# Kernel optimization log

Hardware: AMD Instinct MI355X
Metric: run time of the kernel (lower is better)

## Reference

```python
import jax, jax.numpy as jnp
import numpy as np

IN_DIMS = 512
TOKEN_DIM = 512
NUM_HEADS = 1
D = TOKEN_DIM * NUM_HEADS
SCALE = TOKEN_DIM ** (-0.5)
EPS = 1e-12  # torch F.normalize default


def _l2norm(v, axis):
    n = jnp.sqrt(jnp.sum(v * v, axis=axis, keepdims=True))
    return v / jnp.maximum(n, EPS)


def setup_inputs() -> dict:
    key = jax.random.key(0)
    ks = jax.random.split(key, 10)
    B, C, H, W = 64, IN_DIMS, 28, 28
    s_in = IN_DIMS ** -0.5
    s_d = D ** -0.5
    return {
        "x": jax.random.normal(ks[0], (B, C, H, W), jnp.float32),
        "Wq": jax.random.normal(ks[1], (IN_DIMS, D), jnp.float32) * s_in,
        "bq": jax.random.normal(ks[2], (D,), jnp.float32) * 0.01,
        "Wk": jax.random.normal(ks[3], (IN_DIMS, D), jnp.float32) * s_in,
        "bk": jax.random.normal(ks[4], (D,), jnp.float32) * 0.01,
        "w_g": jax.random.normal(ks[5], (D, 1), jnp.float32),
        "Wp": jax.random.normal(ks[6], (D, D), jnp.float32) * s_d,
        "bp": jax.random.normal(ks[7], (D,), jnp.float32) * 0.01,
        "Wf": jax.random.normal(ks[8], (D, TOKEN_DIM), jnp.float32) * s_d,
        "bf": jax.random.normal(ks[9], (TOKEN_DIM,), jnp.float32) * 0.01,
    }


def reference(x, Wq, bq, Wk, bk, w_g, Wp, bp, Wf, bf):
    B, C, H, W = x.shape
    t = x.reshape(B, C, H * W).transpose(0, 2, 1)          # [B, N, C]
    query = _l2norm(t @ Wq + bq, axis=-1)                  # [B, N, D]
    k = _l2norm(t @ Wk + bk, axis=-1)                      # [B, N, D]
    attn = _l2norm((query @ w_g) * SCALE, axis=1)          # [B, N, 1], normalized over tokens
    ctx = jnp.sum(attn * query, axis=1, keepdims=True)     # [B, 1, D] global context
    out = (ctx * k) @ Wp + bp + query                      # [B, N, D]
    out = out @ Wf + bf                                    # [B, N, TOKEN_DIM]
    return out.transpose(0, 2, 1).reshape(B, -1, H, W)
```

## Files before the change

### kernel.cpp

```cpp
#include <hip/hip_runtime.h>

#define EPSN 1e-12f
#define SCALE_F 0.044194173824159216f
#define MTOT 50176

typedef __bf16 bf16x8 __attribute__((ext_vector_type(8)));
typedef float  f32x4  __attribute__((ext_vector_type(4)));

__device__ __forceinline__ void gld16(const void* src, void* dst) {
  __builtin_amdgcn_global_load_lds(
      (const __attribute__((address_space(1))) unsigned int*)src,
      (__attribute__((address_space(3))) unsigned int*)dst, 16, 0, 0);
}

__global__ __launch_bounds__(256) void k_xt(const float* __restrict__ x,
                                            __bf16* __restrict__ xT, int b0) {
  __shared__ float T[32][33];
  const int n0 = blockIdx.x * 32, c0 = blockIdx.y * 32;
  const int bl = blockIdx.z, b = b0 + bl;
  const int dx = threadIdx.x, ty = threadIdx.y;
  #pragma unroll
  for (int pp = 0; pp < 4; ++pp) {
    int c = ty + pp * 8;
    int n = n0 + dx;
    T[c][dx] = (n < 784) ? x[((size_t)b * 512 + c0 + c) * 784 + n] : 0.f;
  }
  __syncthreads();
  #pragma unroll
  for (int pp = 0; pp < 4; ++pp) {
    int n = ty + pp * 8;
    if (n0 + n < 784)
      xT[((size_t)bl * 784 + n0 + n) * 512 + c0 + dx] = (__bf16)T[dx][n];
  }
}

__global__ __launch_bounds__(256) void k_prep_t(const float* __restrict__ Wq,
                                                const float* __restrict__ Wk,
                                                __bf16* __restrict__ WqT,
                                                __bf16* __restrict__ WkT) {
  __shared__ float Tq[32][33], Tk[32][33];
  const int c0 = blockIdx.x * 32, d0 = blockIdx.y * 32;
  const int dx = threadIdx.x, cy = threadIdx.y;
  #pragma unroll
  for (int p = 0; p < 4; ++p) {
    int c = cy + p * 8;
    Tq[c][dx] = Wq[(size_t)(c0 + c) * 512 + d0 + dx];
    Tk[c][dx] = Wk[(size_t)(c0 + c) * 512 + d0 + dx];
  }
  __syncthreads();
  #pragma unroll
  for (int p = 0; p < 4; ++p) {
    int d = cy + p * 8;
    WqT[(size_t)(d0 + d) * 512 + c0 + dx] = (__bf16)Tq[dx][d];
    WkT[(size_t)(d0 + d) * 512 + c0 + dx] = (__bf16)Tk[dx][d];
  }
}

__global__ __launch_bounds__(512) void k_prep_w(const float* __restrict__ Wp,
                                                const float* __restrict__ Wf,
                                                const float* __restrict__ bp,
                                                const float* __restrict__ bfv,
                                                __bf16* __restrict__ WcT,
                                                float* __restrict__ bpf) {
  const int kk0 = blockIdx.x * 2;
  const int d = threadIdx.x;
  float acc0 = 0.f, acc1 = 0.f, bacc = 0.f;
  const bool dobp = (blockIdx.x == 0);
  for (int c = 0; c < 512; ++c) {
    float wf = Wf[(size_t)c * 512 + d];
    acc0 = fmaf(Wp[(size_t)kk0 * 512 + c],       wf, acc0);
    acc1 = fmaf(Wp[(size_t)(kk0 + 1) * 512 + c], wf, acc1);
    if (dobp) bacc = fmaf(bp[c], wf, bacc);
  }
  WcT[(size_t)d * 1024 + kk0]           = (__bf16)acc0;
  WcT[(size_t)d * 1024 + kk0 + 1]       = (__bf16)acc1;
  WcT[(size_t)d * 1024 + 512 + kk0]     = (__bf16)Wf[(size_t)kk0 * 512 + d];
  WcT[(size_t)d * 1024 + 512 + kk0 + 1] = (__bf16)Wf[(size_t)(kk0 + 1) * 512 + d];
  if (dobp) bpf[d] = bacc + bfv[d];
}

__global__ __launch_bounds__(256, 2) void k_gemm(const __bf16* __restrict__ xT,
                                                 const __bf16* __restrict__ WqT,
                                                 const __bf16* __restrict__ WkT,
                                                 const float* __restrict__ bq,
                                                 const float* __restrict__ bk,
                                                 const float* __restrict__ wg,
                                                 const int b0,
                                                 __bf16* __restrict__ qraw,
                                                 __bf16* __restrict__ kraw,
                                                 float* __restrict__ psqQ,
                                                 float* __restrict__ psqK,
                                                 float* __restrict__ gdo) {
  __shared__ __align__(1024) unsigned char stg[3][24576];
  const int t = threadIdx.x, l = t & 63, w = t >> 6;
  const int li = l & 15, lq = l >> 4;
  const int p = blockIdx.x;
  const int xq = p & 7, q2 = p >> 3;
  const int nt = q2 & 3;
  const int g = (q2 >> 2) * 8 + xq;
  const int bl = g / 7, mt = g % 7;
  const int b = b0 + bl;
  const int m0 = mt * 128;

  const int r0 = 2 * w, r1 = r0 + 1;
  int row0 = m0 + r0 * 16 + li; if (row0 > 783) row0 = 783;
  int row1 = m0 + r1 * 16 + li; if (row1 > 783) row1 = 783;
  const __bf16* a0s = xT + ((size_t)bl * 784 + row0) * 512 + lq * 8;
  const __bf16* a1s = xT + ((size_t)bl * 784 + row1) * 512 + lq * 8;
  const __bf16* q0s = WqT + (size_t)(nt * 128 + r0 * 16 + li) * 512 + lq * 8;
  const __bf16* q1s = WqT + (size_t)(nt * 128 + r1 * 16 + li) * 512 + lq * 8;
  const __bf16* k0s = WkT + (size_t)(nt * 128 + r0 * 16 + li) * 512 + lq * 8;
  const __bf16* k1s = WkT + (size_t)(nt * 128 + r1 * 16 + li) * 512 + lq * 8;

  f32x4 accQ[4][4] = {}, accK[4][4] = {};

  auto stage = [&](unsigned char* buf, int ks) {
    const int kk = (ks > 15 ? 15 : ks) * 32;
    gld16(a0s + kk, buf + r0 * 1024);
    gld16(a1s + kk, buf + r1 * 1024);
    gld16(q0s + kk, buf + 8192 + r0 * 1024);
    gld16(q1s + kk, buf + 8192 + r1 * 1024);
    gld16(k0s + kk, buf + 16384 + r0 * 1024);
    gld16(k1s + kk, buf + 16384 + r1 * 1024);
  };
  auto mstep = [&](const unsigned char* buf) {
    bf16x8 af[4];
    #pragma unroll
    for (int rb = 0; rb < 4; ++rb)
      af[rb] = *(const bf16x8*)(buf + ((w & 1) * 4 + rb) * 1024 + l * 16);
    #pragma unroll
    for (int cb = 0; cb < 4; ++cb) {
      bf16x8 bq8 = *(const bf16x8*)(buf + 8192 + ((w >> 1) * 4 + cb) * 1024 + l * 16);
      #pragma unroll
      for (int rb = 0; rb < 4; ++rb)
        accQ[rb][cb] = __builtin_amdgcn_mfma_f32_16x16x32_bf16(af[rb], bq8, accQ[rb][cb], 0, 0, 0);
      bf16x8 bk8 = *(const bf16x8*)(buf + 16384 + ((w >> 1) * 4 + cb) * 1024 + l * 16);
      #pragma unroll
      for (int rb = 0; rb < 4; ++rb)
        accK[rb][cb] = __builtin_amdgcn_mfma_f32_16x16x32_bf16(af[rb], bk8, accK[rb][cb], 0, 0, 0);
    }
  };

  unsigned char *bc = stg[0], *bn = stg[1], *bn2 = stg[2];
  stage(bc, 0); stage(bn, 1);
  asm volatile("s_waitcnt vmcnt(6)" ::: "memory");
  __builtin_amdgcn_s_barrier();
  __builtin_amdgcn_sched_barrier(0);
  #pragma unroll 1
  for (int ks = 0; ks < 16; ++ks) {
    stage(bn2, ks + 2);
    __builtin_amdgcn_sched_barrier(0);
    mstep(bc);
    asm volatile("s_waitcnt vmcnt(6)" ::: "memory");
    __builtin_amdgcn_s_barrier();
    __builtin_amdgcn_sched_barrier(0);
    unsigned char* tmp = bc; bc = bn; bn = bn2; bn2 = tmp;
  }
  asm volatile("s_waitcnt vmcnt(0)" ::: "memory");

  const int colb = nt * 128 + (w >> 1) * 64;
  const int cg = nt * 2 + (w >> 1);
  float bqv[4], bkv[4], wv[4];
  #pragma unroll
  for (int cb = 0; cb < 4; ++cb) {
    int col = colb + cb * 16 + li;
    bqv[cb] = bq[col]; bkv[cb] = bk[col]; wv[cb] = wg[col];
  }
  #pragma unroll
  for (int rb = 0; rb < 4; ++rb)
    #pragma unroll
    for (int j = 0; j < 4; ++j) {
      int rowg = m0 + (w & 1) * 64 + rb * 16 + lq * 4 + j;
      bool ok = rowg < 784;
      size_t token = (size_t)b * 784 + rowg;
      float ssq = 0.f, ssk = 0.f, sg = 0.f;
      #pragma unroll
      for (int cb = 0; cb < 4; ++cb) {
        float vq = accQ[rb][cb][j] + bqv[cb];
        float vk = accK[rb][cb][j] + bkv[cb];
        ssq = fmaf(vq, vq, ssq);
        ssk = fmaf(vk, vk, ssk);
        sg  = fmaf(vq, wv[cb], sg);
        if (ok) {
          qraw[token * 512 + colb + cb * 16 + li] = (__bf16)vq;
          kraw[token * 512 + colb + cb * 16 + li] = (__bf16)vk;
        }
      }
      ssq += __shfl_xor(ssq, 1); ssq += __shfl_xor(ssq, 2); ssq += __shfl_xor(ssq, 4); ssq += __shfl_xor(ssq, 8);
      ssk += __shfl_xor(ssk, 1); ssk += __shfl_xor(ssk, 2); ssk += __shfl_xor(ssk, 4); ssk += __shfl_xor(ssk, 8);
      sg  += __shfl_xor(sg, 1);  sg  += __shfl_xor(sg, 2);  sg  += __shfl_xor(sg, 4);  sg  += __shfl_xor(sg, 8);
      if (ok && li == 0) {
        psqQ[(size_t)cg * MTOT + token] = ssq;
        psqK[(size_t)cg * MTOT + token] = ssk;
        gdo [(size_t)cg * MTOT + token] = sg;
      }
    }
}

__global__ __launch_bounds__(256) void k_normc(const float* __restrict__ psqQ,
                                               const float* __restrict__ psqK,
                                               const float* __restrict__ gdo,
                                               float* __restrict__ invqA,
                                               float* __restrict__ invkA,
                                               float* __restrict__ coefA,
                                               float* __restrict__ gA) {
  const int tkn = blockIdx.x * 256 + threadIdx.x;
  if (tkn >= MTOT) return;
  float sq = 0.f, sk = 0.f, gd = 0.f;
  #pragma unroll
  for (int cg = 0; cg < 8; ++cg) {
    sq += psqQ[(size_t)cg * MTOT + tkn];
    sk += psqK[(size_t)cg * MTOT + tkn];
    gd += gdo[(size_t)cg * MTOT + tkn];
  }
  float invq = 1.f / fmaxf(sqrtf(sq), EPSN);
  float invk = 1.f / fmaxf(sqrtf(sk), EPSN);
  float gv = gd * invq;
  invqA[tkn] = invq;
  invkA[tkn] = invk;
  coefA[tkn] = gv * invq;
  gA[tkn]    = gv;
}

__global__ __launch_bounds__(512) void k_pctx(const __bf16* __restrict__ qraw,
                                              const float* __restrict__ coefA,
                                              const float* __restrict__ gA,
                                              float* __restrict__ ctx) {
  __shared__ float wred[8];
  __shared__ float part[4][128];
  const int ch = blockIdx.x, b = blockIdx.y, t = threadIdx.x;
  const size_t base = (size_t)b * 784;
  float gsq;
  { float gv = gA[base + t]; gsq = gv * gv; }
  if (t + 512 < 784) { float gv = gA[base + t + 512]; gsq = fmaf(gv, gv, gsq); }
  gsq += __shfl_xor(gsq, 1);  gsq += __shfl_xor(gsq, 2);  gsq += __shfl_xor(gsq, 4);
  gsq += __shfl_xor(gsq, 8);  gsq += __shfl_xor(gsq, 16); gsq += __shfl_xor(gsq, 32);
  if ((t & 63) == 0) wred[t >> 6] = gsq;
  __syncthreads();
  float tot = 0.f;
  #pragma unroll
  for (int i = 0; i < 8; ++i) tot += wred[i];
  const float alpha = SCALE_F / fmaxf(sqrtf(tot) * SCALE_F, EPSN);
  const int dof = t & 127, s = t >> 7;
  const int nb = s * 196;
  const __bf16* qb = qraw + (base + nb) * 512 + ch * 128 + dof;
  const float* cf = coefA + base + nb;
  float a0 = 0.f, a1 = 0.f, a2 = 0.f, a3 = 0.f;
  for (int n = 0; n < 196; n += 4) {
    a0 = fmaf(cf[n],     (float)qb[(size_t)n * 512],       a0);
    a1 = fmaf(cf[n + 1], (float)qb[(size_t)(n + 1) * 512], a1);
    a2 = fmaf(cf[n + 2], (float)qb[(size_t)(n + 2) * 512], a2);
    a3 = fmaf(cf[n + 3], (float)qb[(size_t)(n + 3) * 512], a3);
  }
  part[s][dof] = (a0 + a1) + (a2 + a3);
  __syncthreads();
  if (t < 128) {
    float sum = part[0][t] + part[1][t] + part[2][t] + part[3][t];
    ctx[(size_t)b * 512 + ch * 128 + t] = alpha * sum;
  }
}

__global__ __launch_bounds__(256, 3) void k_out(const __bf16* __restrict__ qraw,
                                                const __bf16* __restrict__ kraw,
                                                const float* __restrict__ invqA,
                                                const float* __restrict__ invkA,
                                                const float* __restrict__ ctx,
                                                const __bf16* __restrict__ WcT,
                                                const float* __restrict__ bpf,
                                                float* __restrict__ out) {
  __shared__ __align__(1024) unsigned char stg[3][16384];
  __shared__ float ctx_l[512];
  const int t = threadIdx.x, l = t & 63, w = t >> 6;
  const int li = l & 15, lq = l >> 4;
  const int p = blockIdx.x;
  const int xq = p & 7, q2 = p >> 3;
  const int nt = q2 & 3;
  const int g = (q2 >> 2) * 8 + xq;
  const int b = g / 7, mt = g % 7;
  const int m0 = mt * 128;

  ctx_l[t]       = ctx[(size_t)b * 512 + t];
  ctx_l[t + 256] = ctx[(size_t)b * 512 + t + 256];
  __syncthreads();

  const int rA0 = w, rA1 = w + 4;
  int row0 = m0 + rA0 * 16 + li; if (row0 > 783) row0 = 783;
  int row1 = m0 + rA1 * 16 + li; if (row1 > 783) row1 = 783;
  const size_t tk0 = (size_t)b * 784 + row0, tk1 = (size_t)b * 784 + row1;
  const float iq0 = invqA[tk0], ik0 = invkA[tk0];
  const float iq1 = invqA[tk1], ik1 = invkA[tk1];
  const __bf16* wpB0 = WcT + (size_t)(nt * 128 + (2 * w) * 16 + li) * 1024 + lq * 8;
  const __bf16* wpB1 = WcT + (size_t)(nt * 128 + (2 * w + 1) * 16 + li) * 1024 + lq * 8;

  f32x4 acc[4][4] = {};

  auto stageB = [&](unsigned char* buf, int ks) {
    const int kk = (ks > 31 ? 31 : ks) * 32;
    gld16(wpB0 + kk, buf + 8192 + (2 * w) * 1024);
    gld16(wpB1 + kk, buf + 8192 + (2 * w + 1) * 1024);
  };
  auto loadA = [&](bf16x8& v0, bf16x8& v1, int ks) {
    const int kk = ks > 31 ? 31 : ks;
    const __bf16* ap = (kk < 16) ? kraw : qraw;
    const int off = (kk & 15) * 32 + lq * 8;
    v0 = *(const bf16x8*)(ap + tk0 * 512 + off);
    v1 = *(const bf16x8*)(ap + tk1 * 512 + off);
  };
  auto writeA = [&](unsigned char* buf, bf16x8 v0, bf16x8 v1, int ks) {
    const int kk = ks > 31 ? 31 : ks;
    bf16x8 o0, o1;
    if (kk < 16) {
      const int kl = (kk & 15) * 32 + lq * 8;
      f32x4 c0 = *(const f32x4*)&ctx_l[kl];
      f32x4 c1 = *(const f32x4*)&ctx_l[kl + 4];
      #pragma unroll
      for (int j = 0; j < 4; ++j) {
        o0[j]     = (__bf16)((float)v0[j]     * ik0 * c0[j]);
        o0[4 + j] = (__bf16)((float)v0[4 + j] * ik0 * c1[j]);
        o1[j]     = (__bf16)((float)v1[j]     * ik1 * c0[j]);
        o1[4 + j] = (__bf16)((float)v1[4 + j] * ik1 * c1[j]);
      }
    } else {
      #pragma unroll
      for (int j = 0; j < 8; ++j) {
        o0[j] = (__bf16)((float)v0[j] * iq0);
        o1[j] = (__bf16)((float)v1[j] * iq1);
      }
    }
    *(bf16x8*)(buf + rA0 * 1024 + l * 16) = o0;
    *(bf16x8*)(buf + rA1 * 1024 + l * 16) = o1;
  };
  auto mstep = [&](const unsigned char* buf) {
    bf16x8 af[4];
    #pragma unroll
    for (int rb = 0; rb < 4; ++rb)
      af[rb] = *(const bf16x8*)(buf + ((w & 1) * 4 + rb) * 1024 + l * 16);
    #pragma unroll
    for (int cb = 0; cb < 4; ++cb) {
      bf16x8 bf = *(const bf16x8*)(buf + 8192 + ((w >> 1) * 4 + cb) * 1024 + l * 16);
      #pragma unroll
      for (int rb = 0; rb < 4; ++rb)
        acc[rb][cb] = __builtin_amdgcn_mfma_f32_16x16x32_bf16(af[rb], bf, acc[rb][cb], 0, 0, 0);
    }
  };

  unsigned char *bc = stg[0], *bn = stg[1], *bn2 = stg[2];
  bf16x8 aA0, aA1, aB0, aB1;
  loadA(aA0, aA1, 0);
  stageB(bc, 0);
  loadA(aB0, aB1, 1);
  stageB(bn, 1);
  asm volatile("s_waitcnt vmcnt(4)" ::: "memory");
  __builtin_amdgcn_sched_barrier(0);
  writeA(bc, aA0, aA1, 0);
  asm volatile("s_waitcnt lgkmcnt(0)" ::: "memory");
  __builtin_amdgcn_s_barrier();
  __builtin_amdgcn_sched_barrier(0);

  #pragma unroll 1
  for (int ks = 0; ks < 32; ks += 2) {
    loadA(aA0, aA1, ks + 2);
    stageB(bn2, ks + 2);
    __builtin_amdgcn_sched_barrier(0);
    mstep(bc);
    asm volatile("s_waitcnt vmcnt(4)" ::: "memory");
    __builtin_amdgcn_sched_barrier(0);
    writeA(bn, aB0, aB1, ks + 1);
    asm volatile("s_waitcnt lgkmcnt(0)" ::: "memory");
    __builtin_amdgcn_s_barrier();
    __builtin_amdgcn_sched_barrier(0);
    loadA(aB0, aB1, ks + 3);
    stageB(bc, ks + 3);
    __builtin_amdgcn_sched_barrier(0);
    mstep(bn);
    asm volatile("s_waitcnt vmcnt(4)" ::: "memory");
    __builtin_amdgcn_sched_barrier(0);
    writeA(bn2, aA0, aA1, ks + 2);
    asm volatile("s_waitcnt lgkmcnt(0)" ::: "memory");
    __builtin_amdgcn_s_barrier();
    __builtin_amdgcn_sched_barrier(0);
    unsigned char* tmp = bc; bc = bn2; bn2 = bn; bn = tmp;
  }
  asm volatile("s_waitcnt vmcnt(0)" ::: "memory");

  const int colb = nt * 128 + (w >> 1) * 64;
  float bv[4];
  #pragma unroll
  for (int cb = 0; cb < 4; ++cb) bv[cb] = bpf[colb + cb * 16 + li];
  #pragma unroll
  for (int rb = 0; rb < 4; ++rb) {
    int nrow = m0 + (w & 1) * 64 + rb * 16 + lq * 4;
    if (nrow < 784) {
      #pragma unroll
      for (int cb = 0; cb < 4; ++cb) {
        f32x4 v;
        #pragma unroll
        for (int j = 0; j < 4; ++j) v[j] = acc[rb][cb][j] + bv[cb];
        *(f32x4*)&out[((size_t)b * 512 + colb + cb * 16 + li) * 784 + nrow] = v;
      }
    }
  }
}

extern "C" void kernel_launch(void* const* d_in, const int* in_sizes, int n_in,
                              void* d_out, int out_size, void* d_ws, size_t ws_size,
                              hipStream_t stream) {
  const float* x   = (const float*)d_in[0];
  const float* Wq  = (const float*)d_in[1];
  const float* bq  = (const float*)d_in[2];
  const float* Wk  = (const float*)d_in[3];
  const float* bk  = (const float*)d_in[4];
  const float* wg  = (const float*)d_in[5];
  const float* Wp  = (const float*)d_in[6];
  const float* bp  = (const float*)d_in[7];
  const float* Wf  = (const float*)d_in[8];
  const float* bfv = (const float*)d_in[9];
  float* out = (float*)d_out;
  char* ws = (char*)d_ws;

  const size_t SZRAW = (size_t)MTOT * 512 * 2;
  const size_t SZXT  = (size_t)32 * 784 * 512 * 2;
  size_t off = 0;
  __bf16* qraw = (__bf16*)(ws + off); off += SZRAW;
  __bf16* kraw = (__bf16*)(ws + off); off += SZRAW;
  __bf16* xT   = (__bf16*)(ws + off); off += SZXT;
  __bf16* WqT  = (__bf16*)(ws + off); off += 524288;
  __bf16* WkT  = (__bf16*)(ws + off); off += 524288;
  __bf16* WcT  = (__bf16*)(ws + off); off += 1048576;
  float*  bpf  = (float*) (ws + off); off += 2048;
  float*  psqQ = (float*) (ws + off); off += (size_t)8 * MTOT * 4;
  float*  psqK = (float*) (ws + off); off += (size_t)8 * MTOT * 4;
  float*  gdo  = (float*) (ws + off); off += (size_t)8 * MTOT * 4;
  float*  invqA = (float*)(ws + off); off += (size_t)MTOT * 4;
  float*  invkA = (float*)(ws + off); off += (size_t)MTOT * 4;
  float*  coefA = (float*)(ws + off); off += (size_t)MTOT * 4;
  float*  gA    = (float*)(ws + off); off += (size_t)MTOT * 4;
  float*  ctx   = (float*)(ws + off); off += 131072;

  k_prep_t<<<dim3(16, 16), dim3(32, 8), 0, stream>>>(Wq, Wk, WqT, WkT);
  k_prep_w<<<dim3(256),    dim3(512),   0, stream>>>(Wp, Wf, bp, bfv, WcT, bpf);
  for (int s = 0; s < 2; ++s) {
    k_xt  <<<dim3(25, 16, 32), dim3(32, 8), 0, stream>>>(x, xT, s * 32);
    k_gemm<<<dim3(896),        dim3(256),   0, stream>>>(xT, WqT, WkT, bq, bk, wg, s * 32,
                                                         qraw, kraw, psqQ, psqK, gdo);
  }
  k_normc<<<dim3(196),   dim3(256), 0, stream>>>(psqQ, psqK, gdo, invqA, invkA, coefA, gA);
  k_pctx <<<dim3(4, 64), dim3(512), 0, stream>>>(qraw, coefA, gA, ctx);
  k_out  <<<dim3(1792),  dim3(256), 0, stream>>>(qraw, kraw, invqA, invkA, ctx, WcT, bpf, out);
}
```

Baseline: 402.5 us.

## Prescale Q and K in separate passes so output GEMM streams A via LDS DMA

Adds two elementwise kernels: one normalizes raw Q in place by its inverse norm, and one scales raw K by its inverse norm times the context vector. The output GEMM then stages both A and B tiles directly with global-to-LDS loads, with no register round-trip or per-element conversion in its main loop, which is simplified to one stage per iteration. This costs an extra read and write pass over both the Q and K buffers (about 100 MB each) and two extra launches, in exchange for a leaner and better-pipelined GEMM inner loop.

```diff
diff --git a/kernel.cpp b/kernel.cpp
--- a/kernel.cpp
+++ b/kernel.cpp
@@ -202,7 +202,6 @@
                                                const float* __restrict__ gdo,
                                                float* __restrict__ invqA,
                                                float* __restrict__ invkA,
-                                               float* __restrict__ coefA,
                                                float* __restrict__ gA) {
   const int tkn = blockIdx.x * 256 + threadIdx.x;
   if (tkn >= MTOT) return;
@@ -215,15 +214,27 @@
   }
   float invq = 1.f / fmaxf(sqrtf(sq), EPSN);
   float invk = 1.f / fmaxf(sqrtf(sk), EPSN);
-  float gv = gd * invq;
   invqA[tkn] = invq;
   invkA[tkn] = invk;
-  coefA[tkn] = gv * invq;
-  gA[tkn]    = gv;
-}
-
-__global__ __launch_bounds__(512) void k_pctx(const __bf16* __restrict__ qraw,
-                                              const float* __restrict__ coefA,
+  gA[tkn]    = gd * invq;
+}
+
+__global__ __launch_bounds__(512) void k_scaleQ(__bf16* __restrict__ qraw,
+                                                const float* __restrict__ invqA) {
+  const int b = blockIdx.y;
+  const int chunk = blockIdx.x * 512 + threadIdx.x;
+  const int row = chunk >> 6;
+  const int c8 = (chunk & 63) * 8;
+  const size_t token = (size_t)b * 784 + row;
+  __bf16* p = qraw + token * 512 + c8;
+  const float s = invqA[token];
+  bf16x8 v = *(const bf16x8*)p;
+  #pragma unroll
+  for (int j = 0; j < 8; ++j) v[j] = (__bf16)((float)v[j] * s);
+  *(bf16x8*)p = v;
+}
+
+__global__ __launch_bounds__(512) void k_pctx(const __bf16* __restrict__ qn,
                                               const float* __restrict__ gA,
                                               float* __restrict__ ctx) {
   __shared__ float wred[8];
@@ -243,8 +254,8 @@
   const float alpha = SCALE_F / fmaxf(sqrtf(tot) * SCALE_F, EPSN);
   const int dof = t & 127, s = t >> 7;
   const int nb = s * 196;
-  const __bf16* qb = qraw + (base + nb) * 512 + ch * 128 + dof;
-  const float* cf = coefA + base + nb;
+  const __bf16* qb = qn + (base + nb) * 512 + ch * 128 + dof;
+  const float* cf = gA + base + nb;
   float a0 = 0.f, a1 = 0.f, a2 = 0.f, a3 = 0.f;
   for (int n = 0; n < 196; n += 4) {
     a0 = fmaf(cf[n],     (float)qb[(size_t)n * 512],       a0);
@@ -260,16 +271,33 @@
   }
 }
 
-__global__ __launch_bounds__(256, 3) void k_out(const __bf16* __restrict__ qraw,
-                                                const __bf16* __restrict__ kraw,
-                                                const float* __restrict__ invqA,
+__global__ __launch_bounds__(512) void k_scaleK(__bf16* __restrict__ kraw,
                                                 const float* __restrict__ invkA,
-                                                const float* __restrict__ ctx,
+                                                const float* __restrict__ ctx) {
+  const int b = blockIdx.y;
+  const int chunk = blockIdx.x * 512 + threadIdx.x;
+  const int row = chunk >> 6;
+  const int c8 = (chunk & 63) * 8;
+  const size_t token = (size_t)b * 784 + row;
+  __bf16* p = kraw + token * 512 + c8;
+  const float s = invkA[token];
+  f32x4 c0 = *(const f32x4*)(ctx + (size_t)b * 512 + c8);
+  f32x4 c1 = *(const f32x4*)(ctx + (size_t)b * 512 + c8 + 4);
+  bf16x8 v = *(const bf16x8*)p;
+  #pragma unroll
+  for (int j = 0; j < 4; ++j) {
+    v[j]     = (__bf16)((float)v[j]     * s * c0[j]);
+    v[4 + j] = (__bf16)((float)v[4 + j] * s * c1[j]);
+  }
+  *(bf16x8*)p = v;
+}
+
+__global__ __launch_bounds__(256, 3) void k_out(const __bf16* __restrict__ qn,
+                                                const __bf16* __restrict__ kc,
                                                 const __bf16* __restrict__ WcT,
                                                 const float* __restrict__ bpf,
                                                 float* __restrict__ out) {
   __shared__ __align__(1024) unsigned char stg[3][16384];
-  __shared__ float ctx_l[512];
   const int t = threadIdx.x, l = t & 63, w = t >> 6;
   const int li = l & 15, lq = l >> 4;
   const int p = blockIdx.x;
@@ -279,56 +307,28 @@
   const int b = g / 7, mt = g % 7;
   const int m0 = mt * 128;
 
-  ctx_l[t]       = ctx[(size_t)b * 512 + t];
-  ctx_l[t + 256] = ctx[(size_t)b * 512 + t + 256];
-  __syncthreads();
-
-  const int rA0 = w, rA1 = w + 4;
-  int row0 = m0 + rA0 * 16 + li; if (row0 > 783) row0 = 783;
-  int row1 = m0 + rA1 * 16 + li; if (row1 > 783) row1 = 783;
+  const int r0 = 2 * w, r1 = r0 + 1;
+  int row0 = m0 + r0 * 16 + li; if (row0 > 783) row0 = 783;
+  int row1 = m0 + r1 * 16 + li; if (row1 > 783) row1 = 783;
   const size_t tk0 = (size_t)b * 784 + row0, tk1 = (size_t)b * 784 + row1;
-  const float iq0 = invqA[tk0], ik0 = invkA[tk0];
-  const float iq1 = invqA[tk1], ik1 = invkA[tk1];
-  const __bf16* wpB0 = WcT + (size_t)(nt * 128 + (2 * w) * 16 + li) * 1024 + lq * 8;
-  const __bf16* wpB1 = WcT + (size_t)(nt * 128 + (2 * w + 1) * 16 + li) * 1024 + lq * 8;
+  const __bf16* ak0 = kc + tk0 * 512 + lq * 8;
+  const __bf16* ak1 = kc + tk1 * 512 + lq * 8;
+  const __bf16* aq0 = qn + tk0 * 512 + lq * 8;
+  const __bf16* aq1 = qn + tk1 * 512 + lq * 8;
+  const __bf16* wpB0 = WcT + (size_t)(nt * 128 + r0 * 16 + li) * 1024 + lq * 8;
+  const __bf16* wpB1 = WcT + (size_t)(nt * 128 + r1 * 16 + li) * 1024 + lq * 8;
 
   f32x4 acc[4][4] = {};
 
-  auto stageB = [&](unsigned char* buf, int ks) {
-    const int kk = (ks > 31 ? 31 : ks) * 32;
-    gld16(wpB0 + kk, buf + 8192 + (2 * w) * 1024);
-    gld16(wpB1 + kk, buf + 8192 + (2 * w + 1) * 1024);
-  };
-  auto loadA = [&](bf16x8& v0, bf16x8& v1, int ks) {
+  auto stage = [&](unsigned char* buf, int ks) {
     const int kk = ks > 31 ? 31 : ks;
-    const __bf16* ap = (kk < 16) ? kraw : qraw;
-    const int off = (kk & 15) * 32 + lq * 8;
-    v0 = *(const bf16x8*)(ap + tk0 * 512 + off);
-    v1 = *(const bf16x8*)(ap + tk1 * 512 + off);
-  };
-  auto writeA = [&](unsigned char* buf, bf16x8 v0, bf16x8 v1, int ks) {
-    const int kk = ks > 31 ? 31 : ks;
-    bf16x8 o0, o1;
-    if (kk < 16) {
-      const int kl = (kk & 15) * 32 + lq * 8;
-      f32x4 c0 = *(const f32x4*)&ctx_l[kl];
-      f32x4 c1 = *(const f32x4*)&ctx_l[kl + 4];
-      #pragma unroll
-      for (int j = 0; j < 4; ++j) {
-        o0[j]     = (__bf16)((float)v0[j]     * ik0 * c0[j]);
-        o0[4 + j] = (__bf16)((float)v0[4 + j] * ik0 * c1[j]);
-        o1[j]     = (__bf16)((float)v1[j]     * ik1 * c0[j]);
-        o1[4 + j] = (__bf16)((float)v1[4 + j] * ik1 * c1[j]);
-      }
-    } else {
-      #pragma unroll
-      for (int j = 0; j < 8; ++j) {
-        o0[j] = (__bf16)((float)v0[j] * iq0);
-        o1[j] = (__bf16)((float)v1[j] * iq1);
-      }
-    }
-    *(bf16x8*)(buf + rA0 * 1024 + l * 16) = o0;
-    *(bf16x8*)(buf + rA1 * 1024 + l * 16) = o1;
+    const int off = (kk & 15) * 32;
+    const __bf16* s0 = (kk < 16) ? ak0 : aq0;
+    const __bf16* s1 = (kk < 16) ? ak1 : aq1;
+    gld16(s0 + off, buf + r0 * 1024);
+    gld16(s1 + off, buf + r1 * 1024);
+    gld16(wpB0 + kk * 32, buf + 8192 + r0 * 1024);
+    gld16(wpB1 + kk * 32, buf + 8192 + r1 * 1024);
   };
   auto mstep = [&](const unsigned char* buf) {
     bf16x8 af[4];
@@ -345,41 +345,19 @@
   };
 
   unsigned char *bc = stg[0], *bn = stg[1], *bn2 = stg[2];
-  bf16x8 aA0, aA1, aB0, aB1;
-  loadA(aA0, aA1, 0);
-  stageB(bc, 0);
-  loadA(aB0, aB1, 1);
-  stageB(bn, 1);
+  stage(bc, 0); stage(bn, 1);
   asm volatile("s_waitcnt vmcnt(4)" ::: "memory");
-  __builtin_amdgcn_sched_barrier(0);
-  writeA(bc, aA0, aA1, 0);
-  asm volatile("s_waitcnt lgkmcnt(0)" ::: "memory");
   __builtin_amdgcn_s_barrier();
   __builtin_amdgcn_sched_barrier(0);
-
   #pragma unroll 1
-  for (int ks = 0; ks < 32; ks += 2) {
-    loadA(aA0, aA1, ks + 2);
-    stageB(bn2, ks + 2);
+  for (int ks = 0; ks < 32; ++ks) {
+    stage(bn2, ks + 2);
     __builtin_amdgcn_sched_barrier(0);
     mstep(bc);
     asm volatile("s_waitcnt vmcnt(4)" ::: "memory");
-    __builtin_amdgcn_sched_barrier(0);
-    writeA(bn, aB0, aB1, ks + 1);
-    asm volatile("s_waitcnt lgkmcnt(0)" ::: "memory");
     __builtin_amdgcn_s_barrier();
     __builtin_amdgcn_sched_barrier(0);
-    loadA(aB0, aB1, ks + 3);
-    stageB(bc, ks + 3);
-    __builtin_amdgcn_sched_barrier(0);
-    mstep(bn);
-    asm volatile("s_waitcnt vmcnt(4)" ::: "memory");
-    __builtin_amdgcn_sched_barrier(0);
-    writeA(bn2, aA0, aA1, ks + 2);
-    asm volatile("s_waitcnt lgkmcnt(0)" ::: "memory");
-    __builtin_amdgcn_s_barrier();
-    __builtin_amdgcn_sched_barrier(0);
-    unsigned char* tmp = bc; bc = bn2; bn2 = bn; bn = tmp;
+    unsigned char* tmp = bc; bc = bn; bn = bn2; bn2 = tmp;
   }
   asm volatile("s_waitcnt vmcnt(0)" ::: "memory");
 
@@ -433,7 +411,6 @@
   float*  gdo  = (float*) (ws + off); off += (size_t)8 * MTOT * 4;
   float*  invqA = (float*)(ws + off); off += (size_t)MTOT * 4;
   float*  invkA = (float*)(ws + off); off += (size_t)MTOT * 4;
-  float*  coefA = (float*)(ws + off); off += (size_t)MTOT * 4;
   float*  gA    = (float*)(ws + off); off += (size_t)MTOT * 4;
   float*  ctx   = (float*)(ws + off); off += 131072;
 
@@ -444,7 +421,9 @@
     k_gemm<<<dim3(896),        dim3(256),   0, stream>>>(xT, WqT, WkT, bq, bk, wg, s * 32,
                                                          qraw, kraw, psqQ, psqK, gdo);
   }
-  k_normc<<<dim3(196),   dim3(256), 0, stream>>>(psqQ, psqK, gdo, invqA, invkA, coefA, gA);
-  k_pctx <<<dim3(4, 64), dim3(512), 0, stream>>>(qraw, coefA, gA, ctx);
-  k_out  <<<dim3(1792),  dim3(256), 0, stream>>>(qraw, kraw, invqA, invkA, ctx, WcT, bpf, out);
-}
+  k_normc <<<dim3(196),    dim3(256), 0, stream>>>(psqQ, psqK, gdo, invqA, invkA, gA);
+  k_scaleQ<<<dim3(98, 64), dim3(512), 0, stream>>>(qraw, invqA);
+  k_pctx  <<<dim3(4, 64),  dim3(512), 0, stream>>>(qraw, gA, ctx);
+  k_scaleK<<<dim3(98, 64), dim3(512), 0, stream>>>(kraw, invkA, ctx);
+  k_out   <<<dim3(1792),   dim3(256), 0, stream>>>(qraw, kraw, WcT, bpf, out);
+}
```

After: 421.5 us. +4.7%, slower.
